# Kernel optimization log

Hardware: AMD Instinct MI355X
Metric: run time of the kernel (lower is better)

Reference implementation:

```python
import jax, jax.numpy as jnp
import numpy as np

DIM = 1024
E = 8
HID = 4 * DIM  # DomainExpert FFN hidden size


def setup_inputs() -> dict:
    key = jax.random.key(0)
    ks = jax.random.split(key, 7)
    x = jax.random.normal(ks[0], (1, 2048, DIM), dtype=jnp.float32)
    Wr = jax.random.normal(ks[1], (DIM, E), dtype=jnp.float32) * (DIM ** -0.5)
    br = jnp.zeros((E,), dtype=jnp.float32)
    W1 = jax.random.normal(ks[2], (E, DIM, HID), dtype=jnp.float32) * (DIM ** -0.5)
    b1 = jnp.zeros((E, 1, HID), dtype=jnp.float32)
    W2 = jax.random.normal(ks[3], (E, HID, DIM), dtype=jnp.float32) * (HID ** -0.5)
    b2 = jnp.zeros((E, 1, DIM), dtype=jnp.float32)
    return {"x": x, "Wr": Wr, "br": br, "W1": W1, "b1": b1, "W2": W2, "b2": b2}


def reference(x, Wr, br, W1, b1, W2, b2):
    B, T, D = x.shape
    flat = x.reshape(B * T, D)                       # [N, D]
    logits = flat @ Wr + br                          # [N, E]
    z_loss = jnp.mean(jax.nn.logsumexp(logits, axis=-1) ** 2)
    probs = jax.nn.softmax(logits, axis=-1)          # eval path (no Gumbel)
    top_p, top_i = jax.lax.top_k(probs, 2)           # [N, 2]
    top_p = top_p / (top_p.sum(-1, keepdims=True) + 1e-12)
    N = flat.shape[0]
    nE = Wr.shape[1]
    # combine weights: w[t, e] = renormalized top-2 prob if e selected, else 0
    w = jnp.zeros((N, nE), dtype=flat.dtype).at[
        jnp.arange(N)[:, None], top_i].add(top_p)   # [N, E]
    # dense (jit-friendly) expert compute; combine masks out unselected experts
    h = jax.nn.gelu(jnp.einsum('td,edh->teh', flat, W1) + b1.transpose(1, 0, 2))  # [N, E, HID]
    y = jnp.einsum('teh,ehd->ted', h, W2) + b2.transpose(1, 0, 2)                 # [N, E, D]
    out = jnp.einsum('ted,te->td', y, w).reshape(B, T, D)
    importance = probs.mean(axis=0)                                               # [E]
    fi = jax.nn.one_hot(top_i, nE, dtype=flat.dtype).sum(axis=1).mean(axis=0)     # [E]
    aux_loss = jnp.asarray(nE, flat.dtype) * (importance * fi).sum()
    return out, z_loss, aux_loss
```

## Files before the change

### kernel.cpp

```cpp
#include <hip/hip_runtime.h>
#include <math.h>

#define N_TOK 2048
#define DIM   1024
#define NEXP  8
#define HID   4096
#define TOTPAIR (2 * N_TOK)

#define BM 128
#define BN 128
#define BK 32
#define LDST 40

typedef __bf16 bf16x8 __attribute__((ext_vector_type(8)));
typedef __bf16 bf16x4 __attribute__((ext_vector_type(4)));
typedef float  f32x4  __attribute__((ext_vector_type(4)));

__device__ __forceinline__ float gelu_tanh(float v) {
    float a = 0.7978845608028654f * (v + 0.044715f * v * v * v);
    a = fminf(fmaxf(a, -15.f), 15.f);
    float t = __expf(-2.f * a);
    return 0.5f * v * (1.f + (1.f - t) / (1.f + t));
}

__global__ void router_kernel(const float* __restrict__ x, const float* __restrict__ Wr,
                              const float* __restrict__ br,
                              float* __restrict__ probs, float* __restrict__ lsq,
                              int* __restrict__ cnt, int* __restrict__ tok,
                              float* __restrict__ wl) {
    const int t = blockIdx.x;
    const int lane = threadIdx.x;
    const float* xr = x + (size_t)t * DIM;
    float acc[NEXP];
#pragma unroll
    for (int e = 0; e < NEXP; e++) acc[e] = 0.f;
    for (int d = lane; d < DIM; d += 64) {
        float xv = xr[d];
        const float* wr = Wr + (size_t)d * NEXP;
#pragma unroll
        for (int e = 0; e < NEXP; e++) acc[e] = fmaf(xv, wr[e], acc[e]);
    }
#pragma unroll
    for (int off = 32; off >= 1; off >>= 1) {
#pragma unroll
        for (int e = 0; e < NEXP; e++) acc[e] += __shfl_xor(acc[e], off, 64);
    }
    if (lane == 0) {
        float lg[NEXP], mx = -1e30f;
#pragma unroll
        for (int e = 0; e < NEXP; e++) { lg[e] = acc[e] + br[e]; mx = fmaxf(mx, lg[e]); }
        float se = 0.f, p[NEXP];
#pragma unroll
        for (int e = 0; e < NEXP; e++) { p[e] = expf(lg[e] - mx); se += p[e]; }
        float inv = 1.f / se;
        float lse = mx + logf(se);
        lsq[t] = lse * lse;
#pragma unroll
        for (int e = 0; e < NEXP; e++) probs[t * NEXP + e] = p[e] * inv;
        int i0 = 0;
#pragma unroll
        for (int e = 1; e < NEXP; e++) if (p[e] > p[i0]) i0 = e;
        int i1 = (i0 == 0) ? 1 : 0;
#pragma unroll
        for (int e = 0; e < NEXP; e++) if (e != i0 && p[e] > p[i1]) i1 = e;
        float p0 = p[i0] * inv, p1 = p[i1] * inv;
        float rn = 1.f / (p0 + p1 + 1e-12f);
        int pos0 = atomicAdd(&cnt[i0], 1);
        tok[i0 * N_TOK + pos0] = t;
        wl[i0 * N_TOK + pos0] = p0 * rn;
        int pos1 = atomicAdd(&cnt[i1], 1);
        tok[i1 * N_TOK + pos1] = t;
        wl[i1 * N_TOK + pos1] = p1 * rn;
    }
}

__global__ void offsets_kernel(const int* __restrict__ cnt, int* __restrict__ offs) {
    if (threadIdx.x == 0) {
        int s = 0;
        for (int e = 0; e < NEXP; e++) { offs[e] = s; s += cnt[e]; }
    }
}

__global__ void conv_x_kernel(const float* __restrict__ x, __bf16* __restrict__ xb) {
    int idx = blockIdx.x * 256 + threadIdx.x;
    float4 v = ((const float4*)x)[idx];
    bf16x4 o;
    o.x = (__bf16)v.x; o.y = (__bf16)v.y; o.z = (__bf16)v.z; o.w = (__bf16)v.w;
    ((bf16x4*)xb)[idx] = o;
}

__global__ __launch_bounds__(256) void transpose_conv_kernel(
    const float* __restrict__ in, __bf16* __restrict__ out, int R, int C) {
    __shared__ __bf16 tile[32][33];
    const int tx = threadIdx.x & 31, ty = threadIdx.x >> 5;
    const size_t eoff = (size_t)blockIdx.z * (size_t)R * (size_t)C;
    const int rb = blockIdx.y * 32, cb = blockIdx.x * 32;
#pragma unroll
    for (int i = 0; i < 4; i++) {
        int r = rb + ty + i * 8;
        tile[ty + i * 8][tx] = (__bf16)in[eoff + (size_t)r * C + cb + tx];
    }
    __syncthreads();
#pragma unroll
    for (int i = 0; i < 4; i++) {
        int c = cb + ty + i * 8;
        out[eoff + (size_t)c * R + rb + tx] = tile[tx][ty + i * 8];
    }
}

__global__ __launch_bounds__(256, 4) void gemm1_kernel(
    const __bf16* __restrict__ xb, const __bf16* __restrict__ W1T,
    const float* __restrict__ b1,
    const int* __restrict__ cnt, const int* __restrict__ offs,
    const int* __restrict__ tok, __bf16* __restrict__ h) {
    const int e = blockIdx.z;
    const int ce = cnt[e];
    const int mstart = blockIdx.y * BM;
    if (mstart >= ce) return;
    const int n0 = blockIdx.x * BN;

    __shared__ __bf16 As[BM][LDST];
    __shared__ __bf16 Bs[BN][LDST];
    __shared__ int toksh[BM];

    const int tid = threadIdx.x;
    if (tid < BM) {
        int idx = mstart + tid;
        toksh[tid] = (idx < ce) ? tok[e * N_TOK + idx] : 0;
    }
    __syncthreads();

    const int lane = tid & 63;
    const int wid  = tid >> 6;
    const int row0 = (wid >> 1) * 64;
    const int col0 = (wid & 1) * 64;
    const int quad = lane >> 4;
    const int lcol = lane & 15;
    const int srow = tid >> 2;
    const int sk   = (tid & 3) * 8;

    const __bf16* __restrict__ W1e = W1T + (size_t)e * HID * DIM;

    f32x4 acc[4][4];
#pragma unroll
    for (int i = 0; i < 4; i++)
#pragma unroll
        for (int j = 0; j < 4; j++) acc[i][j] = (f32x4){0.f, 0.f, 0.f, 0.f};

    for (int k0 = 0; k0 < DIM; k0 += BK) {
#pragma unroll
        for (int p = 0; p < 2; p++) {
            int r = p * 64 + srow;
            *(bf16x8*)&As[r][sk] = *(const bf16x8*)(xb + (size_t)toksh[r] * DIM + k0 + sk);
            *(bf16x8*)&Bs[r][sk] = *(const bf16x8*)(W1e + (size_t)(n0 + r) * DIM + k0 + sk);
        }
        __syncthreads();
        bf16x8 af[4], bfr[4];
#pragma unroll
        for (int i = 0; i < 4; i++) af[i]  = *(const bf16x8*)&As[row0 + i * 16 + lcol][quad * 8];
#pragma unroll
        for (int j = 0; j < 4; j++) bfr[j] = *(const bf16x8*)&Bs[col0 + j * 16 + lcol][quad * 8];
#pragma unroll
        for (int i = 0; i < 4; i++)
#pragma unroll
            for (int j = 0; j < 4; j++)
                acc[i][j] = __builtin_amdgcn_mfma_f32_16x16x32_bf16(af[i], bfr[j], acc[i][j], 0, 0, 0);
        __syncthreads();
    }

    const float* __restrict__ b1e = b1 + (size_t)e * HID;
    const int offe = offs[e];
#pragma unroll
    for (int i = 0; i < 4; i++) {
#pragma unroll
        for (int reg = 0; reg < 4; reg++) {
            int pos = mstart + row0 + i * 16 + quad * 4 + reg;
            if (pos >= ce) continue;
            size_t hbase = (size_t)(offe + pos) * HID;
#pragma unroll
            for (int j = 0; j < 4; j++) {
                int gcol = n0 + col0 + j * 16 + lcol;
                float v = acc[i][j][reg] + b1e[gcol];
                h[hbase + gcol] = (__bf16)gelu_tanh(v);
            }
        }
    }
}

__global__ __launch_bounds__(256, 4) void gemm2_kernel(
    const __bf16* __restrict__ h, const __bf16* __restrict__ W2T,
    const float* __restrict__ b2,
    const int* __restrict__ cnt, const int* __restrict__ offs,
    const int* __restrict__ tok, const float* __restrict__ wl,
    float* __restrict__ out) {
    const int e = blockIdx.z;
    const int ce = cnt[e];
    const int mstart = blockIdx.y * BM;
    if (mstart >= ce) return;
    const int n0 = blockIdx.x * BN;

    __shared__ __bf16 As[BM][LDST];
    __shared__ __bf16 Bs[BN][LDST];
    __shared__ int   toksh[BM];
    __shared__ float wsh[BM];

    const int tid = threadIdx.x;
    if (tid < BM) {
        int idx = mstart + tid;
        toksh[tid] = (idx < ce) ? tok[e * N_TOK + idx] : 0;
        wsh[tid]   = (idx < ce) ? wl[e * N_TOK + idx] : 0.f;
    }

    const int lane = tid & 63;
    const int wid  = tid >> 6;
    const int row0 = (wid >> 1) * 64;
    const int col0 = (wid & 1) * 64;
    const int quad = lane >> 4;
    const int lcol = lane & 15;
    const int srow = tid >> 2;
    const int sk   = (tid & 3) * 8;

    const int offe = offs[e];
    const __bf16* __restrict__ W2e = W2T + (size_t)e * DIM * HID;

    f32x4 acc[4][4];
#pragma unroll
    for (int i = 0; i < 4; i++)
#pragma unroll
        for (int j = 0; j < 4; j++) acc[i][j] = (f32x4){0.f, 0.f, 0.f, 0.f};

    for (int k0 = 0; k0 < HID; k0 += BK) {
#pragma unroll
        for (int p = 0; p < 2; p++) {
            int r = p * 64 + srow;
            int hr = offe + mstart + r;
            hr = (hr < TOTPAIR) ? hr : (TOTPAIR - 1);
            *(bf16x8*)&As[r][sk] = *(const bf16x8*)(h + (size_t)hr * HID + k0 + sk);
            *(bf16x8*)&Bs[r][sk] = *(const bf16x8*)(W2e + (size_t)(n0 + r) * HID + k0 + sk);
        }
        __syncthreads();
        bf16x8 af[4], bfr[4];
#pragma unroll
        for (int i = 0; i < 4; i++) af[i]  = *(const bf16x8*)&As[row0 + i * 16 + lcol][quad * 8];
#pragma unroll
        for (int j = 0; j < 4; j++) bfr[j] = *(const bf16x8*)&Bs[col0 + j * 16 + lcol][quad * 8];
#pragma unroll
        for (int i = 0; i < 4; i++)
#pragma unroll
            for (int j = 0; j < 4; j++)
                acc[i][j] = __builtin_amdgcn_mfma_f32_16x16x32_bf16(af[i], bfr[j], acc[i][j], 0, 0, 0);
        __syncthreads();
    }

    const float* __restrict__ b2e = b2 + (size_t)e * DIM;
#pragma unroll
    for (int i = 0; i < 4; i++) {
#pragma unroll
        for (int reg = 0; reg < 4; reg++) {
            int lrow = row0 + i * 16 + quad * 4 + reg;
            int pos = mstart + lrow;
            if (pos >= ce) continue;
            int tokm = toksh[lrow];
            float w = wsh[lrow];
#pragma unroll
            for (int j = 0; j < 4; j++) {
                int gcol = n0 + col0 + j * 16 + lcol;
                float v = acc[i][j][reg] + b2e[gcol];
                atomicAdd(&out[(size_t)tokm * DIM + gcol], w * v);
            }
        }
    }
}

__global__ __launch_bounds__(256, 2) void ffn_fallback_kernel(
    const float* __restrict__ x,
    const float* __restrict__ W1, const float* __restrict__ b1,
    const float* __restrict__ W2, const float* __restrict__ b2,
    const int* __restrict__ cnt, const int* __restrict__ tok,
    const float* __restrict__ wl, float* __restrict__ out) {
    const int e = blockIdx.y;
    const int ce = cnt[e];
    const int start = blockIdx.x * 16;
    if (start >= ce) return;
    __shared__ float hs[16][128];
    __shared__ int toks[16];
    __shared__ float wgt[16];
    const int tid = threadIdx.x;
    if (tid < 16) {
        int idx = start + tid;
        if (idx < ce) { toks[tid] = tok[e * N_TOK + idx]; wgt[tid] = wl[e * N_TOK + idx]; }
        else          { toks[tid] = -1;                   wgt[tid] = 0.f; }
    }
    __syncthreads();
    const float* __restrict__ W1e = W1 + (size_t)e * DIM * HID;
    const float* __restrict__ W2e = W2 + (size_t)e * HID * DIM;
    const int am  = tid >> 4;
    const int aj0 = (tid & 15) * 8;
    const int at  = toks[am];
    const float* __restrict__ xrow = x + (size_t)(at < 0 ? 0 : at) * DIM;
    const int n0 = tid * 4;
    float acc[16][4];
#pragma unroll
    for (int m = 0; m < 16; m++)
#pragma unroll
        for (int i = 0; i < 4; i++) acc[m][i] = 0.f;
    for (int c = 0; c < HID; c += 128) {
        float ha[8];
#pragma unroll
        for (int r = 0; r < 8; r++) ha[r] = 0.f;
        const float* wp = W1e + c + aj0;
        for (int d = 0; d < DIM; d += 4) {
            float4 xv = *(const float4*)(xrow + d);
#pragma unroll
            for (int k = 0; k < 4; k++) {
                const float* wr = wp + (size_t)(d + k) * HID;
                float4 wa = *(const float4*)(wr);
                float4 wb = *(const float4*)(wr + 4);
                float xk = (k == 0) ? xv.x : (k == 1) ? xv.y : (k == 2) ? xv.z : xv.w;
                ha[0] = fmaf(xk, wa.x, ha[0]); ha[1] = fmaf(xk, wa.y, ha[1]);
                ha[2] = fmaf(xk, wa.z, ha[2]); ha[3] = fmaf(xk, wa.w, ha[3]);
                ha[4] = fmaf(xk, wb.x, ha[4]); ha[5] = fmaf(xk, wb.y, ha[5]);
                ha[6] = fmaf(xk, wb.z, ha[6]); ha[7] = fmaf(xk, wb.w, ha[7]);
            }
        }
        __syncthreads();
#pragma unroll
        for (int r = 0; r < 8; r++) {
            float v = ha[r] + b1[e * HID + c + aj0 + r];
            hs[am][aj0 + r] = gelu_tanh(v);
        }
        __syncthreads();
        for (int jj = 0; jj < 128; jj++) {
            float4 wv = *(const float4*)(W2e + (size_t)(c + jj) * DIM + n0);
#pragma unroll
            for (int m = 0; m < 16; m++) {
                float hv = hs[m][jj];
                acc[m][0] = fmaf(hv, wv.x, acc[m][0]); acc[m][1] = fmaf(hv, wv.y, acc[m][1]);
                acc[m][2] = fmaf(hv, wv.z, acc[m][2]); acc[m][3] = fmaf(hv, wv.w, acc[m][3]);
            }
        }
    }
    const float* bp = b2 + e * DIM + n0;
    float b0 = bp[0], b1v = bp[1], b2v = bp[2], b3 = bp[3];
#pragma unroll 1
    for (int m = 0; m < 16; m++) {
        int t = toks[m];
        if (t < 0) continue;
        float w = wgt[m];
        float* op = out + (size_t)t * DIM + n0;
        atomicAdd(op + 0, w * (acc[m][0] + b0));
        atomicAdd(op + 1, w * (acc[m][1] + b1v));
        atomicAdd(op + 2, w * (acc[m][2] + b2v));
        atomicAdd(op + 3, w * (acc[m][3] + b3));
    }
}

__global__ void finalize_kernel(const float* __restrict__ probs, const float* __restrict__ lsq,
                                const int* __restrict__ cnt, float* __restrict__ scal) {
    __shared__ float part[256][9];
    const int tid = threadIdx.x;
    float z = 0.f;
    float im[NEXP];
#pragma unroll
    for (int e = 0; e < NEXP; e++) im[e] = 0.f;
    for (int t = tid; t < N_TOK; t += 256) {
        z += lsq[t];
#pragma unroll
        for (int e = 0; e < NEXP; e++) im[e] += probs[t * NEXP + e];
    }
    part[tid][0] = z;
#pragma unroll
    for (int e = 0; e < NEXP; e++) part[tid][1 + e] = im[e];
    __syncthreads();
    if (tid == 0) {
        float zs = 0.f, ims[NEXP];
        for (int e = 0; e < NEXP; e++) ims[e] = 0.f;
        for (int i = 0; i < 256; i++) {
            zs += part[i][0];
            for (int e = 0; e < NEXP; e++) ims[e] += part[i][1 + e];
        }
        float nInv = 1.0f / (float)N_TOK;
        float aux = 0.f;
        for (int e = 0; e < NEXP; e++) aux += (ims[e] * nInv) * ((float)cnt[e] * nInv);
        scal[0] = zs * nInv;
        scal[1] = (float)NEXP * aux;
    }
}

extern "C" void kernel_launch(void* const* d_in, const int* in_sizes, int n_in,
                              void* d_out, int out_size, void* d_ws, size_t ws_size,
                              hipStream_t stream) {
    const float* x  = (const float*)d_in[0];
    const float* Wr = (const float*)d_in[1];
    const float* br = (const float*)d_in[2];
    const float* W1 = (const float*)d_in[3];
    const float* b1 = (const float*)d_in[4];
    const float* W2 = (const float*)d_in[5];
    const float* b2 = (const float*)d_in[6];
    float* out = (float*)d_out;

    char* base = (char*)d_ws;
    int*   cnt   = (int*)(base);
    int*   offs  = (int*)(base + 32);
    int*   tokp  = (int*)(base + 64);
    float* wlp   = (float*)(base + 64 + 65536);
    float* probs = (float*)(base + 64 + 2 * 65536);
    float* lsq   = (float*)(base + 64 + 3 * 65536);
    const size_t SMALL_END = 64 + 3 * 65536 + 8192;
    __bf16* xb   = (__bf16*)(base + SMALL_END);
    __bf16* W1T  = (__bf16*)(base + SMALL_END + 4194304ull);
    __bf16* W2T  = (__bf16*)(base + SMALL_END + 4194304ull + 67108864ull);
    __bf16* hbuf = (__bf16*)(base + SMALL_END + 4194304ull + 2ull * 67108864ull);
    const size_t REQ = SMALL_END + 4194304ull + 2ull * 67108864ull + 33554432ull;

    hipMemsetAsync(base, 0, 64, stream);
    hipMemsetAsync(d_out, 0, (size_t)out_size * sizeof(float), stream);

    router_kernel<<<N_TOK, 64, 0, stream>>>(x, Wr, br, probs, lsq, cnt, tokp, wlp);

    if (ws_size >= REQ) {
        offsets_kernel<<<1, 1, 0, stream>>>(cnt, offs);
        conv_x_kernel<<<(N_TOK * DIM / 4) / 256, 256, 0, stream>>>(x, xb);
        transpose_conv_kernel<<<dim3(HID / 32, DIM / 32, NEXP), 256, 0, stream>>>(W1, W1T, DIM, HID);
        transpose_conv_kernel<<<dim3(DIM / 32, HID / 32, NEXP), 256, 0, stream>>>(W2, W2T, HID, DIM);
        gemm1_kernel<<<dim3(HID / BN, N_TOK / BM, NEXP), 256, 0, stream>>>(
            xb, W1T, b1, cnt, offs, tokp, hbuf);
        gemm2_kernel<<<dim3(DIM / BN, N_TOK / BM, NEXP), 256, 0, stream>>>(
            hbuf, W2T, b2, cnt, offs, tokp, wlp, out);
    } else {
        ffn_fallback_kernel<<<dim3(128, NEXP), 256, 0, stream>>>(
            x, W1, b1, W2, b2, cnt, tokp, wlp, out);
    }

    finalize_kernel<<<1, 256, 0, stream>>>(probs, lsq, cnt, out + (size_t)N_TOK * DIM);
}
```

Measured before the change: 664.6 us.

## Use direct global-to-LDS loads with swizzle, split-K gemm2, vectorize weight transpose

Three separate changes. The GEMM kernels now stage tiles with global_load_lds direct-to-LDS copies into an XOR-swizzled, unpadded layout, which removes register round trips and should avoid LDS bank conflicts. gemm2 is split four ways along K, so more blocks run on the GPU; each partial sum is added to the output with atomics, and only the first split adds the bias. The transpose-convert kernel moves to 64x64 tiles with float4 reads and 16-byte writes. The costs are four times the atomic traffic on the output and a dependence on the builtin's lane-addressing semantics being correct.

Result: faster. 586.7 us (-11.7%).

```diff
diff --git a/kernel.cpp b/kernel.cpp
--- a/kernel.cpp
+++ b/kernel.cpp
@@ -10,7 +10,7 @@
 #define BM 128
 #define BN 128
 #define BK 32
-#define LDST 40
+#define KSPLIT2 4
 
 typedef __bf16 bf16x8 __attribute__((ext_vector_type(8)));
 typedef __bf16 bf16x4 __attribute__((ext_vector_type(4)));
@@ -21,6 +21,16 @@
     a = fminf(fmaxf(a, -15.f), 15.f);
     float t = __expf(-2.f * a);
     return 0.5f * v * (1.f + (1.f - t) / (1.f + t));
+}
+
+__device__ __forceinline__ void stage16(const __bf16* g, __bf16* lds_base, int lane) {
+#if defined(__has_builtin) && __has_builtin(__builtin_amdgcn_global_load_lds)
+    __builtin_amdgcn_global_load_lds((const __attribute__((address_space(1))) void*)g,
+                                     (__attribute__((address_space(3))) void*)lds_base,
+                                     16, 0, 0);
+#else
+    *(bf16x8*)((char*)lds_base + (size_t)lane * 16) = *(const bf16x8*)g;
+#endif
 }
 
 __global__ void router_kernel(const float* __restrict__ x, const float* __restrict__ Wr,
@@ -91,20 +101,28 @@
 
 __global__ __launch_bounds__(256) void transpose_conv_kernel(
     const float* __restrict__ in, __bf16* __restrict__ out, int R, int C) {
-    __shared__ __bf16 tile[32][33];
-    const int tx = threadIdx.x & 31, ty = threadIdx.x >> 5;
+    __shared__ __bf16 tile[64][68];
+    const int t = threadIdx.x;
     const size_t eoff = (size_t)blockIdx.z * (size_t)R * (size_t)C;
-    const int rb = blockIdx.y * 32, cb = blockIdx.x * 32;
+    const int rb = blockIdx.y * 64, cb = blockIdx.x * 64;
+    const int r = t >> 4, c4 = (t & 15) * 4;
 #pragma unroll
     for (int i = 0; i < 4; i++) {
-        int r = rb + ty + i * 8;
-        tile[ty + i * 8][tx] = (__bf16)in[eoff + (size_t)r * C + cb + tx];
+        int row = r + i * 16;
+        float4 v = *(const float4*)(in + eoff + (size_t)(rb + row) * C + cb + c4);
+        bf16x4 o;
+        o.x = (__bf16)v.x; o.y = (__bf16)v.y; o.z = (__bf16)v.z; o.w = (__bf16)v.w;
+        *(bf16x4*)&tile[row][c4] = o;
     }
     __syncthreads();
-#pragma unroll
-    for (int i = 0; i < 4; i++) {
-        int c = cb + ty + i * 8;
-        out[eoff + (size_t)c * R + rb + tx] = tile[tx][ty + i * 8];
+    const int c = t >> 2, ch0 = t & 3;
+#pragma unroll
+    for (int i = 0; i < 2; i++) {
+        int ch = ch0 + i * 4;
+        bf16x8 o;
+#pragma unroll
+        for (int j = 0; j < 8; j++) o[j] = tile[ch * 8 + j][c];
+        *(bf16x8*)(out + eoff + (size_t)(cb + c) * R + rb + ch * 8) = o;
     }
 }
 
@@ -119,8 +137,8 @@
     if (mstart >= ce) return;
     const int n0 = blockIdx.x * BN;
 
-    __shared__ __bf16 As[BM][LDST];
-    __shared__ __bf16 Bs[BN][LDST];
+    __shared__ __bf16 As[BM * BK];
+    __shared__ __bf16 Bs[BN * BK];
     __shared__ int toksh[BM];
 
     const int tid = threadIdx.x;
@@ -136,10 +154,25 @@
     const int col0 = (wid & 1) * 64;
     const int quad = lane >> 4;
     const int lcol = lane & 15;
-    const int srow = tid >> 2;
-    const int sk   = (tid & 3) * 8;
+
+    const int sub = lane >> 2;
+    const int gk  = (((lane & 3) ^ (sub & 3)) << 3);
+    const int ra0 = wid * 32 + sub;
+    const int ra1 = ra0 + 16;
 
     const __bf16* __restrict__ W1e = W1T + (size_t)e * HID * DIM;
+    const __bf16* pA0 = xb + (size_t)toksh[ra0] * DIM + gk;
+    const __bf16* pA1 = xb + (size_t)toksh[ra1] * DIM + gk;
+    const __bf16* pB0 = W1e + (size_t)(n0 + ra0) * DIM + gk;
+    const __bf16* pB1 = W1e + (size_t)(n0 + ra1) * DIM + gk;
+    __bf16* lA0 = &As[(wid * 2 + 0) * 512];
+    __bf16* lA1 = &As[(wid * 2 + 1) * 512];
+    __bf16* lB0 = &Bs[(wid * 2 + 0) * 512];
+    __bf16* lB1 = &Bs[(wid * 2 + 1) * 512];
+
+    const int swz = (quad ^ (lcol & 3)) << 3;
+    const __bf16* aF = &As[(row0 + lcol) * BK + swz];
+    const __bf16* bF = &Bs[(col0 + lcol) * BK + swz];
 
     f32x4 acc[4][4];
 #pragma unroll
@@ -148,18 +181,16 @@
         for (int j = 0; j < 4; j++) acc[i][j] = (f32x4){0.f, 0.f, 0.f, 0.f};
 
     for (int k0 = 0; k0 < DIM; k0 += BK) {
-#pragma unroll
-        for (int p = 0; p < 2; p++) {
-            int r = p * 64 + srow;
-            *(bf16x8*)&As[r][sk] = *(const bf16x8*)(xb + (size_t)toksh[r] * DIM + k0 + sk);
-            *(bf16x8*)&Bs[r][sk] = *(const bf16x8*)(W1e + (size_t)(n0 + r) * DIM + k0 + sk);
-        }
+        stage16(pA0 + k0, lA0, lane);
+        stage16(pA1 + k0, lA1, lane);
+        stage16(pB0 + k0, lB0, lane);
+        stage16(pB1 + k0, lB1, lane);
         __syncthreads();
         bf16x8 af[4], bfr[4];
 #pragma unroll
-        for (int i = 0; i < 4; i++) af[i]  = *(const bf16x8*)&As[row0 + i * 16 + lcol][quad * 8];
-#pragma unroll
-        for (int j = 0; j < 4; j++) bfr[j] = *(const bf16x8*)&Bs[col0 + j * 16 + lcol][quad * 8];
+        for (int i = 0; i < 4; i++) af[i]  = *(const bf16x8*)(aF + i * 16 * BK);
+#pragma unroll
+        for (int j = 0; j < 4; j++) bfr[j] = *(const bf16x8*)(bF + j * 16 * BK);
 #pragma unroll
         for (int i = 0; i < 4; i++)
 #pragma unroll
@@ -193,14 +224,16 @@
     const int* __restrict__ cnt, const int* __restrict__ offs,
     const int* __restrict__ tok, const float* __restrict__ wl,
     float* __restrict__ out) {
-    const int e = blockIdx.z;
+    const int e = blockIdx.z >> 2;
+    const int split = blockIdx.z & 3;
     const int ce = cnt[e];
     const int mstart = blockIdx.y * BM;
     if (mstart >= ce) return;
     const int n0 = blockIdx.x * BN;
-
-    __shared__ __bf16 As[BM][LDST];
-    __shared__ __bf16 Bs[BN][LDST];
+    const int ks = split * (HID / KSPLIT2);
+
+    __shared__ __bf16 As[BM * BK];
+    __shared__ __bf16 Bs[BN * BK];
     __shared__ int   toksh[BM];
     __shared__ float wsh[BM];
 
@@ -210,6 +243,7 @@
         toksh[tid] = (idx < ce) ? tok[e * N_TOK + idx] : 0;
         wsh[tid]   = (idx < ce) ? wl[e * N_TOK + idx] : 0.f;
     }
+    __syncthreads();
 
     const int lane = tid & 63;
     const int wid  = tid >> 6;
@@ -217,11 +251,29 @@
     const int col0 = (wid & 1) * 64;
     const int quad = lane >> 4;
     const int lcol = lane & 15;
-    const int srow = tid >> 2;
-    const int sk   = (tid & 3) * 8;
+
+    const int sub = lane >> 2;
+    const int gk  = (((lane & 3) ^ (sub & 3)) << 3);
+    const int ra0 = wid * 32 + sub;
+    const int ra1 = ra0 + 16;
 
     const int offe = offs[e];
+    int hr0 = offe + mstart + ra0; if (hr0 >= TOTPAIR) hr0 = TOTPAIR - 1;
+    int hr1 = offe + mstart + ra1; if (hr1 >= TOTPAIR) hr1 = TOTPAIR - 1;
+
     const __bf16* __restrict__ W2e = W2T + (size_t)e * DIM * HID;
+    const __bf16* pA0 = h + (size_t)hr0 * HID + ks + gk;
+    const __bf16* pA1 = h + (size_t)hr1 * HID + ks + gk;
+    const __bf16* pB0 = W2e + (size_t)(n0 + ra0) * HID + ks + gk;
+    const __bf16* pB1 = W2e + (size_t)(n0 + ra1) * HID + ks + gk;
+    __bf16* lA0 = &As[(wid * 2 + 0) * 512];
+    __bf16* lA1 = &As[(wid * 2 + 1) * 512];
+    __bf16* lB0 = &Bs[(wid * 2 + 0) * 512];
+    __bf16* lB1 = &Bs[(wid * 2 + 1) * 512];
+
+    const int swz = (quad ^ (lcol & 3)) << 3;
+    const __bf16* aF = &As[(row0 + lcol) * BK + swz];
+    const __bf16* bF = &Bs[(col0 + lcol) * BK + swz];
 
     f32x4 acc[4][4];
 #pragma unroll
@@ -229,21 +281,17 @@
 #pragma unroll
         for (int j = 0; j < 4; j++) acc[i][j] = (f32x4){0.f, 0.f, 0.f, 0.f};
 
-    for (int k0 = 0; k0 < HID; k0 += BK) {
-#pragma unroll
-        for (int p = 0; p < 2; p++) {
-            int r = p * 64 + srow;
-            int hr = offe + mstart + r;
-            hr = (hr < TOTPAIR) ? hr : (TOTPAIR - 1);
-            *(bf16x8*)&As[r][sk] = *(const bf16x8*)(h + (size_t)hr * HID + k0 + sk);
-            *(bf16x8*)&Bs[r][sk] = *(const bf16x8*)(W2e + (size_t)(n0 + r) * HID + k0 + sk);
-        }
+    for (int k0 = 0; k0 < HID / KSPLIT2; k0 += BK) {
+        stage16(pA0 + k0, lA0, lane);
+        stage16(pA1 + k0, lA1, lane);
+        stage16(pB0 + k0, lB0, lane);
+        stage16(pB1 + k0, lB1, lane);
         __syncthreads();
         bf16x8 af[4], bfr[4];
 #pragma unroll
-        for (int i = 0; i < 4; i++) af[i]  = *(const bf16x8*)&As[row0 + i * 16 + lcol][quad * 8];
-#pragma unroll
-        for (int j = 0; j < 4; j++) bfr[j] = *(const bf16x8*)&Bs[col0 + j * 16 + lcol][quad * 8];
+        for (int i = 0; i < 4; i++) af[i]  = *(const bf16x8*)(aF + i * 16 * BK);
+#pragma unroll
+        for (int j = 0; j < 4; j++) bfr[j] = *(const bf16x8*)(bF + j * 16 * BK);
 #pragma unroll
         for (int i = 0; i < 4; i++)
 #pragma unroll
@@ -253,6 +301,7 @@
     }
 
     const float* __restrict__ b2e = b2 + (size_t)e * DIM;
+    const bool addBias = (split == 0);
 #pragma unroll
     for (int i = 0; i < 4; i++) {
 #pragma unroll
@@ -265,7 +314,7 @@
 #pragma unroll
             for (int j = 0; j < 4; j++) {
                 int gcol = n0 + col0 + j * 16 + lcol;
-                float v = acc[i][j][reg] + b2e[gcol];
+                float v = acc[i][j][reg] + (addBias ? b2e[gcol] : 0.f);
                 atomicAdd(&out[(size_t)tokm * DIM + gcol], w * v);
             }
         }
@@ -421,11 +470,11 @@
     if (ws_size >= REQ) {
         offsets_kernel<<<1, 1, 0, stream>>>(cnt, offs);
         conv_x_kernel<<<(N_TOK * DIM / 4) / 256, 256, 0, stream>>>(x, xb);
-        transpose_conv_kernel<<<dim3(HID / 32, DIM / 32, NEXP), 256, 0, stream>>>(W1, W1T, DIM, HID);
-        transpose_conv_kernel<<<dim3(DIM / 32, HID / 32, NEXP), 256, 0, stream>>>(W2, W2T, HID, DIM);
+        transpose_conv_kernel<<<dim3(HID / 64, DIM / 64, NEXP), 256, 0, stream>>>(W1, W1T, DIM, HID);
+        transpose_conv_kernel<<<dim3(DIM / 64, HID / 64, NEXP), 256, 0, stream>>>(W2, W2T, HID, DIM);
         gemm1_kernel<<<dim3(HID / BN, N_TOK / BM, NEXP), 256, 0, stream>>>(
             xb, W1T, b1, cnt, offs, tokp, hbuf);
-        gemm2_kernel<<<dim3(DIM / BN, N_TOK / BM, NEXP), 256, 0, stream>>>(
+        gemm2_kernel<<<dim3(DIM / BN, N_TOK / BM, NEXP * KSPLIT2), 256, 0, stream>>>(
             hbuf, W2T, b2, cnt, offs, tokp, wlp, out);
     } else {
         ffn_fallback_kernel<<<dim3(128, NEXP), 256, 0, stream>>>(
```
